# Optimization experiments

Hardware: AMD Instinct MI355X
Metric: run time of the kernel (lower is better)

## Reference

```python
import jax, jax.numpy as jnp
import numpy as np
from jax import lax

VOCAB = 28996  # bert-base-cased vocab size (static for segment_sum)
B, S, D = 32, 512, 768
NUM_CLASSES = 9


def _lstm_dir(x, w_ih, w_hh, b_ih, b_hh):
    # x: [T, N, In]; torch gate order i, f, g, o packed along dim 0 of weights
    T, N, _ = x.shape
    H = w_hh.shape[1]
    xg = jnp.einsum('tni,gi->tng', x, w_ih) + b_ih  # precompute input projections [T,N,4H]

    def step(carry, xg_t):
        h, c = carry
        g = xg_t + h @ w_hh.T + b_hh
        i, f, gg, o = jnp.split(g, 4, axis=-1)
        c = jax.nn.sigmoid(f) * c + jax.nn.sigmoid(i) * jnp.tanh(gg)
        h = jax.nn.sigmoid(o) * jnp.tanh(c)
        return (h, c), h

    h0 = jnp.zeros((N, H), x.dtype)
    _, ys = lax.scan(step, (h0, h0), xg)
    return ys  # [T, N, H]


def setup_inputs() -> dict:
    key = jax.random.key(0)
    ks = jax.random.split(key, 8)
    H, In = D, 2 * D
    w = 0.02
    return {
        'batch': jax.random.randint(ks[0], (B, S), 0, VOCAB),
        'hidden': jax.random.normal(ks[1], (B, S, D), jnp.float32),
        'w_ih_f': jax.random.normal(ks[2], (4 * H, In), jnp.float32) * w,
        'w_hh_f': jax.random.normal(ks[3], (4 * H, H), jnp.float32) * w,
        'b_ih_f': jnp.zeros((4 * H,), jnp.float32),
        'b_hh_f': jnp.zeros((4 * H,), jnp.float32),
        'w_ih_b': jax.random.normal(ks[4], (4 * H, In), jnp.float32) * w,
        'w_hh_b': jax.random.normal(ks[5], (4 * H, H), jnp.float32) * w,
        'b_ih_b': jnp.zeros((4 * H,), jnp.float32),
        'b_hh_b': jnp.zeros((4 * H,), jnp.float32),
        'lin_w': jax.random.normal(ks[6], (NUM_CLASSES, 2 * H), jnp.float32) * w,
        'lin_b': jnp.zeros((NUM_CLASSES,), jnp.float32),
    }


def reference(batch, hidden, w_ih_f, w_hh_f, b_ih_f, b_hh_f,
              w_ih_b, w_hh_b, b_ih_b, b_hh_b, lin_w, lin_b):
    b, s, d = hidden.shape
    flat_ids = batch.reshape(-1)            # [B*S]
    flat_h = hidden.reshape(-1, d)          # [B*S, D]
    # segment mean of embeddings grouped by raw token id (the dict loop in torch)
    sums = jax.ops.segment_sum(flat_h, flat_ids, num_segments=VOCAB)
    counts = jax.ops.segment_sum(jnp.ones((flat_ids.shape[0], 1), hidden.dtype),
                                 flat_ids, num_segments=VOCAB)
    means = sums / jnp.maximum(counts, 1.0)
    ctx = means[flat_ids].reshape(b, s, d)  # gather-broadcast back per position
    x = jnp.concatenate([hidden, ctx], axis=2)  # [B, S, 2D]
    # nn.LSTM is not batch_first: scans over dim0 (B acts as time, S as batch)
    out_f = _lstm_dir(x, w_ih_f, w_hh_f, b_ih_f, b_hh_f)
    out_b = _lstm_dir(x[::-1], w_ih_b, w_hh_b, b_ih_b, b_hh_b)[::-1]
    out = jnp.concatenate([out_f, out_b], axis=-1)  # [B, S, 2D]
    # dropout is identity in eval mode
    return out @ lin_w.T + lin_b  # [B, S, num_classes]
```

## Files before the change

### kernel.cpp

```cpp
#include <hip/hip_runtime.h>

#define VOCAB 28996
#define BB 32
#define SS 512
#define DD 768
#define NCLS 9
#define ROWS (BB*SS)
#define IN2 (2*DD)
#define G4 (4*DD)
#define NB2 (2*G4)

typedef __attribute__((ext_vector_type(8))) short short8;
typedef __attribute__((ext_vector_type(4))) short shortx4;
typedef __attribute__((ext_vector_type(4))) float floatx4;
typedef unsigned long long ull;

__device__ __forceinline__ float bf2f(unsigned short u){
  union { unsigned int i; float f; } v; v.i = ((unsigned int)u) << 16; return v.f;
}
__device__ __forceinline__ unsigned short f2bf(float f){
  union { float f; unsigned int i; } v; v.f = f;
  unsigned int r = v.i + 0x7FFFu + ((v.i >> 16) & 1u);
  return (unsigned short)(r >> 16);
}
__device__ __forceinline__ float sigf(float x){ return 1.0f / (1.0f + __expf(-x)); }
__device__ __forceinline__ float tanhfast(float x){
  float y = fminf(fmaxf(x, -15.f), 15.f);
  float e = __expf(2.f * y);
  return 1.f - 2.f / (e + 1.f);
}

__device__ __forceinline__ void gl_lds16(const unsigned short* g, unsigned short* l){
  __builtin_amdgcn_global_load_lds((__attribute__((address_space(1))) void*)(g),
                                   (__attribute__((address_space(3))) void*)(l), 16, 0, 0);
}
__device__ __forceinline__ void gl_lds16_c(const unsigned short* g, unsigned short* l){
  __builtin_amdgcn_global_load_lds((__attribute__((address_space(1))) void*)(g),
                                   (__attribute__((address_space(3))) void*)(l), 16, 0, 17);
}
__device__ __forceinline__ void store16_sc1(unsigned short* p, short8 v){
  asm volatile("global_store_dwordx4 %0, %1, off sc0 sc1" :: "v"(p), "v"(v) : "memory");
}

#define VMCNT(n) do { asm volatile("s_waitcnt vmcnt(" #n ")" ::: "memory"); \
                      __builtin_amdgcn_sched_barrier(0); } while (0)

__global__ void seg_scatter(const int* __restrict__ ids, const float* __restrict__ hidden,
                            float* __restrict__ sums, float* __restrict__ counts)
{
  int r = blockIdx.x;
  int id = ids[r];
  const float* h = hidden + (long)r * DD;
  float* s = sums + (long)id * DD;
  for (int d = threadIdx.x; d < DD; d += 256)
    atomicAdd(&s[d], h[d]);
  if (threadIdx.x == 0) atomicAdd(&counts[id], 1.0f);
}

__global__ void build_x(const int* __restrict__ ids, const float* __restrict__ hidden,
                        const float* __restrict__ sums, const float* __restrict__ counts,
                        unsigned short* __restrict__ x)
{
  int r = blockIdx.x;
  int id = ids[r];
  float inv = 1.0f / fmaxf(counts[id], 1.0f);
  const float* h = hidden + (long)r * DD;
  const float* s = sums + (long)id * DD;
  unsigned short* xr = x + (long)r * IN2;
  for (int d = threadIdx.x; d < DD; d += 256) {
    xr[d]      = f2bf(h[d]);
    xr[DD + d] = f2bf(s[d] * inv);
  }
}

__global__ void conv_w_perm(const float* __restrict__ w, unsigned short* __restrict__ o, int K)
{
  long i = (long)blockIdx.x * 256 + threadIdx.x;
  if (i >= (long)G4 * K) return;
  int row = (int)(i / K); int k = (int)(i - (long)row * K);
  int u = row >> 2, g = row & 3;
  o[i] = f2bf(w[((long)(g * DD + u)) * K + k]);
}

__global__ void conv_bias_perm(const float* __restrict__ bif, const float* __restrict__ bhf,
                               const float* __restrict__ bib, const float* __restrict__ bhb,
                               float* __restrict__ o)
{
  int n = blockIdx.x * 256 + threadIdx.x;
  if (n >= NB2) return;
  int d = n / G4, rr = n - d * G4, u = rr >> 2, g = rr & 3;
  int s = g * DD + u;
  o[n] = d ? (bib[s] + bhb[s]) : (bif[s] + bhf[s]);
}

__global__ __launch_bounds__(512, 1)
void gemm_bt256(const unsigned short* __restrict__ A, int lda,
                const unsigned short* __restrict__ B, int ldb,
                unsigned short* __restrict__ C, int ldc,
                const float* __restrict__ bias, int K)
{
  __shared__ unsigned short lA[2][16384];
  __shared__ unsigned short lB[2][16384];
  const int t = threadIdx.x;
  const int lane = t & 63;
  const int wv = t >> 6;
  const int wm = wv >> 1;
  const int wn = wv & 1;
  const int l15 = lane & 15, q = lane >> 4;
  const long m0 = (long)blockIdx.x * 256;
  const long n0 = (long)blockIdx.y * 256;
  const int rs  = t >> 2;
  const int sc  = (((t & 3) ^ ((t >> 3) & 3))) * 8;
  const int qsw = (q ^ ((l15 >> 1) & 3)) * 8;

  const unsigned short* gA = A + (m0 + rs) * (long)lda + sc;
  const unsigned short* gB = B + (n0 + rs) * (long)ldb + sc;
  const long a128 = (long)128 * lda;
  const long b128 = (long)128 * ldb;

  #define PIECE(b, kt, p, hf) do {                                               \
    const long kb_ = (long)(kt) * 64 + (p) * 32 + (hf) * 0;                      \
    gl_lds16(gA + kb_ + (hf) * a128, &lA[b][(p) * 8192 + (hf) * 4096 + t * 8]);  \
    gl_lds16(gB + kb_ + (hf) * b128, &lB[b][(p) * 8192 + (hf) * 4096 + t * 8]);  \
  } while (0)

  floatx4 acc[4][8];
  #pragma unroll
  for (int i = 0; i < 4; i++)
    #pragma unroll
    for (int j = 0; j < 8; j++)
      acc[i][j] = (floatx4){0.f, 0.f, 0.f, 0.f};

  PIECE(0, 0, 0, 0); PIECE(0, 0, 0, 1);
  PIECE(0, 0, 1, 0); PIECE(0, 0, 1, 1);

  #pragma unroll 2
  for (int kt = 0; kt < 24; kt++) {
    const int cur = kt & 1;
    const int nxt = cur ^ 1;
    const unsigned short* pA = &lA[cur][0];
    const unsigned short* pB = &lB[cur][0];

    VMCNT(4);
    __builtin_amdgcn_s_barrier();

    #pragma unroll
    for (int ks = 0; ks < 2; ks++) {
      short8 bfr[8];
      #pragma unroll
      for (int ih = 0; ih < 2; ih++) {
        if (kt < 23) {
          if (ks == 0 && ih == 0) PIECE(nxt, kt + 1, 0, 0);
          if (ks == 0 && ih == 1) PIECE(nxt, kt + 1, 0, 1);
          if (ks == 1 && ih == 0) PIECE(nxt, kt + 1, 1, 0);
          if (ks == 1 && ih == 1) PIECE(nxt, kt + 1, 1, 1);
        }
        if (ih == 0) {
          #pragma unroll
          for (int j = 0; j < 8; j++)
            bfr[j] = *(const short8*)(pB + ks * 8192 + (wn * 128 + j * 16 + l15) * 32 + qsw);
        }
        short8 af[2];
        #pragma unroll
        for (int ii = 0; ii < 2; ii++)
          af[ii] = *(const short8*)(pA + ks * 8192 + (wm * 64 + (ih * 2 + ii) * 16 + l15) * 32 + qsw);
        __builtin_amdgcn_s_setprio(1);
        #pragma unroll
        for (int ii = 0; ii < 2; ii++)
          #pragma unroll
          for (int j = 0; j < 8; j++)
            acc[ih * 2 + ii][j] =
              __builtin_amdgcn_mfma_f32_16x16x32_bf16(af[ii], bfr[j], acc[ih * 2 + ii][j], 0, 0, 0);
        __builtin_amdgcn_s_setprio(0);
      }
      if (ks == 0) {
        if (kt < 23) VMCNT(4); else VMCNT(0);
        __builtin_amdgcn_s_barrier();
      }
    }
  }
  #undef PIECE

  #pragma unroll
  for (int i = 0; i < 4; i++) {
    #pragma unroll
    for (int j = 0; j < 8; j++) {
      const long mg = m0 + wm * 64 + i * 16 + q * 4;
      const long ng = n0 + wn * 128 + j * 16 + l15;
      const float bb = bias[ng];
      #pragma unroll
      for (int r = 0; r < 4; r++)
        C[(mg + r) * (long)ldc + ng] = f2bf(acc[i][j][r] + bb);
    }
  }
}

__global__ __launch_bounds__(512, 1)
void lstm_persist(const unsigned short* __restrict__ xg, int ldxg,
                  const unsigned short* __restrict__ whh,
                  unsigned short* __restrict__ hbuf,
                  unsigned short* __restrict__ outc,
                  unsigned* bar,
                  int dir0, int ndir)
{
  __shared__ unsigned short bufA[2][16384];
  __shared__ unsigned short bufB[2][16384];
  __shared__ unsigned short hout[128 * 40];

  const int bid = blockIdx.x;
  const int xcd = bid & 7;
  const int idx = bid >> 3;
  int dm, k3;
  if (ndir == 2) { dm = idx & 7; k3 = idx >> 3; }
  else           { dm = idx & 3; k3 = idx >> 2; }
  const int ld  = (ndir == 2) ? (dm & 1) : 0;
  const int dir = dir0 + ld;
  const int mt  = (ndir == 2) ? (dm >> 1) : dm;
  const int nt  = k3 * 8 + xcd;
  const int m0 = mt * 128, n0 = nt * 128;
  const int u0 = n0 >> 2;
  unsigned* gbar = bar + dm * 16;
  const int nb24 = 24;

  const int t0 = threadIdx.x;
  const int lane = t0 & 63;
  const int wv = t0 >> 6;
  const int wm = wv >> 1;
  const int wn = wv & 1;
  const int l15 = lane & 15, q = lane >> 4;
  const long ldoff = (ndir == 2 && ld == 1) ? (long)G4 : 0;

  const unsigned short* Bdir = whh + (long)dir * G4 * DD;
  const int srow  = lane >> 2;
  const int scolA = (((lane & 3) ^ ((lane >> 3) & 3))) * 8;
  const int qsw   = (q ^ ((l15 >> 1) & 3)) * 8;

  const int rb = wv * 16 + srow;
  const unsigned short* wB  = Bdir + (long)(n0 + rb) * DD + scolA;
  const unsigned short* hA0 = hbuf + ((long)0 * ndir + ld) * ((long)SS * DD) + (long)(m0 + rb) * DD + scolA;
  const unsigned short* hA1 = hbuf + ((long)1 * ndir + ld) * ((long)SS * DD) + (long)(m0 + rb) * DD + scolA;

  float c_reg[2][4];
  #pragma unroll
  for (int i = 0; i < 2; i++)
    #pragma unroll
    for (int j = 0; j < 4; j++)
      c_reg[i][j] = 0.f;

  for (int s = 0; s < BB; s++) {
    const int tt = dir ? (BB - 1 - s) : s;
    const unsigned short* hA = (s & 1) ? hA1 : hA0;
    unsigned short* hw = hbuf + (((long)((s + 1) & 1)) * ndir + ld) * ((long)SS * DD);

    #pragma unroll
    for (int p = 0; p < 4; p++) {
      gl_lds16_c(hA + p * 32, &bufA[0][p * 4096 + wv * 512 + lane * 8]);
      gl_lds16 (wB + p * 32, &bufB[0][p * 4096 + wv * 512 + lane * 8]);
    }
    shortx4 xr0[4], xr1[4];
    {
      const unsigned short* xb = xg + ((long)tt * SS + m0) * ldxg + ldoff + n0;
      const unsigned short* xb0 = xb + (long)(wm * 32 + l15) * ldxg + wn * 64 + q * 4;
      const unsigned short* xb1 = xb0 + (long)16 * ldxg;
      #pragma unroll
      for (int j = 0; j < 4; j++) {
        xr0[j] = *(const shortx4*)(xb0 + j * 16);
        xr1[j] = *(const shortx4*)(xb1 + j * 16);
      }
    }

    floatx4 acc[2][4];
    #pragma unroll
    for (int i = 0; i < 2; i++)
      #pragma unroll
      for (int j = 0; j < 4; j++)
        acc[i][j] = (floatx4){0.f, 0.f, 0.f, 0.f};

    #pragma unroll
    for (int j6 = 0; j6 < 6; j6++) {
      if (j6 < 5) {
        const int b = (j6 + 1) & 1;
        const long kb = (long)(j6 + 1) * 128;
        #pragma unroll
        for (int p = 0; p < 4; p++) {
          gl_lds16_c(hA + kb + p * 32, &bufA[b][p * 4096 + wv * 512 + lane * 8]);
          gl_lds16 (wB + kb + p * 32, &bufB[b][p * 4096 + wv * 512 + lane * 8]);
        }
      }
      if (j6 == 0)      VMCNT(16);
      else if (j6 < 5)  VMCNT(8);
      else              VMCNT(0);
      __builtin_amdgcn_s_barrier();
      const int b = j6 & 1;
      __builtin_amdgcn_s_setprio(1);
      #pragma unroll
      for (int ks = 0; ks < 4; ks++) {
        const unsigned short* pA = &bufA[b][ks * 4096];
        const unsigned short* pB = &bufB[b][ks * 4096];
        short8 af[2], bfr[4];
        #pragma unroll
        for (int i = 0; i < 2; i++)
          af[i] = *(const short8*)(pA + (wm * 32 + i * 16 + l15) * 32 + qsw);
        #pragma unroll
        for (int j = 0; j < 4; j++)
          bfr[j] = *(const short8*)(pB + (wn * 64 + j * 16 + l15) * 32 + qsw);
        #pragma unroll
        for (int i = 0; i < 2; i++)
          #pragma unroll
          for (int j = 0; j < 4; j++)
            acc[i][j] = __builtin_amdgcn_mfma_f32_16x16x32_bf16(bfr[j], af[i], acc[i][j], 0, 0, 0);
      }
      __builtin_amdgcn_s_setprio(0);
      if (j6 < 5) __builtin_amdgcn_s_barrier();
    }

    #pragma unroll
    for (int i = 0; i < 2; i++) {
      const int mrow = wm * 32 + i * 16 + l15;
      #pragma unroll
      for (int j = 0; j < 4; j++) {
        const int nb = wn * 64 + j * 16 + q * 4;
        shortx4 xv = i ? xr1[j] : xr0[j];
        float gi = acc[i][j][0] + bf2f((unsigned short)xv[0]);
        float gf = acc[i][j][1] + bf2f((unsigned short)xv[1]);
        float gg = acc[i][j][2] + bf2f((unsigned short)xv[2]);
        float go = acc[i][j][3] + bf2f((unsigned short)xv[3]);
        float c = sigf(gf) * c_reg[i][j] + sigf(gi) * tanhfast(gg);
        float h = sigf(go) * tanhfast(c);
        c_reg[i][j] = c;
        hout[mrow * 40 + (nb >> 2)] = f2bf(h);
      }
    }
    __syncthreads();
    {
      const int row = t0 >> 2;
      const int qq = t0 & 3;
      short8 v0 = *(const short8*)(hout + row * 40 + qq * 8);
      unsigned short* hwp = hw + (long)(m0 + row) * DD + u0 + qq * 8;
      unsigned short* op  = outc + ((long)tt * SS + m0 + row) * IN2 + dir * DD + u0 + qq * 8;
      store16_sc1(hwp, v0);
      *(short8*)op = v0;
    }
    if (s < BB - 1) {
      VMCNT(0);
      __builtin_amdgcn_s_barrier();
      if (threadIdx.x == 0) {
        unsigned g = __hip_atomic_load(gbar + 1, __ATOMIC_RELAXED, __HIP_MEMORY_SCOPE_AGENT);
        unsigned a = __hip_atomic_fetch_add(gbar, 1u, __ATOMIC_RELAXED, __HIP_MEMORY_SCOPE_AGENT);
        if (a == (unsigned)(nb24 - 1)) {
          __hip_atomic_store(gbar, 0u, __ATOMIC_RELAXED, __HIP_MEMORY_SCOPE_AGENT);
          __hip_atomic_store(gbar + 1, g + 1u, __ATOMIC_RELEASE, __HIP_MEMORY_SCOPE_AGENT);
        } else {
          unsigned curv;
          do {
            __builtin_amdgcn_s_sleep(2);
            curv = __hip_atomic_load(gbar + 1, __ATOMIC_RELAXED, __HIP_MEMORY_SCOPE_AGENT);
          } while (curv == g);
        }
      }
      __builtin_amdgcn_s_barrier();
    }
  }
}

__global__ void final_linear(const unsigned short* __restrict__ xin, const float* __restrict__ w,
                             const float* __restrict__ b, float* __restrict__ out)
{
  __shared__ float red[NCLS * 256];
  int row = blockIdx.x;
  const unsigned short* x = xin + (long)row * IN2;
  float p[NCLS];
  #pragma unroll
  for (int c = 0; c < NCLS; c++) p[c] = 0.f;
  for (int k = threadIdx.x; k < IN2; k += 256) {
    float xv = bf2f(x[k]);
    #pragma unroll
    for (int c = 0; c < NCLS; c++) p[c] += xv * w[c * IN2 + k];
  }
  #pragma unroll
  for (int c = 0; c < NCLS; c++) red[c * 256 + threadIdx.x] = p[c];
  __syncthreads();
  for (int s = 128; s > 0; s >>= 1) {
    if (threadIdx.x < s) {
      #pragma unroll
      for (int c = 0; c < NCLS; c++)
        red[c * 256 + threadIdx.x] += red[c * 256 + threadIdx.x + s];
    }
    __syncthreads();
  }
  if (threadIdx.x < NCLS)
    out[(long)row * NCLS + threadIdx.x] = red[threadIdx.x * 256] + b[threadIdx.x];
}

extern "C" void kernel_launch(void* const* d_in, const int* in_sizes, int n_in,
                              void* d_out, int out_size, void* d_ws, size_t ws_size,
                              hipStream_t stream)
{
  const int*   batch  = (const int*)d_in[0];
  const float* hidden = (const float*)d_in[1];
  const float* w_ih_f = (const float*)d_in[2];
  const float* w_hh_f = (const float*)d_in[3];
  const float* b_ih_f = (const float*)d_in[4];
  const float* b_hh_f = (const float*)d_in[5];
  const float* w_ih_b = (const float*)d_in[6];
  const float* w_hh_b = (const float*)d_in[7];
  const float* b_ih_b = (const float*)d_in[8];
  const float* b_hh_b = (const float*)d_in[9];
  const float* lin_w  = (const float*)d_in[10];
  const float* lin_b  = (const float*)d_in[11];
  float* out = (float*)d_out;

  char* ws = (char*)d_ws;
  size_t off = 0;
  auto alloc = [&](size_t bytes) -> char* {
    char* p = ws + off;
    off += (bytes + 255) & ~(size_t)255;
    return p;
  };

  const size_t SZ_XG_A = (size_t)ROWS * NB2 * 2;
  const size_t SZ_XG_B = (size_t)ROWS * G4  * 2;
  const size_t SZ_XBF  = (size_t)ROWS * IN2 * 2;
  const size_t SZ_W    = (size_t)G4 * IN2 * 2;
  const size_t SZ_BIAS = (size_t)NB2 * 4;
  const size_t SZ_HBUF = (size_t)2 * 2 * SS * DD * 2;
  const size_t SZ_BAR  = 512;
  const size_t SZ_SUMS = (size_t)VOCAB * DD * 4 + (size_t)VOCAB * 4;

  const size_t NEED_C = SZ_XG_A + SZ_XBF + SZ_W + SZ_BIAS + SZ_HBUF + SZ_BAR + 8 * 256;
  const bool combined = ws_size >= NEED_C;

  const long nWIH = (long)G4 * IN2;
  const long nWHH = (long)G4 * DD;

  if (combined) {
    unsigned short* xg   = (unsigned short*)alloc(SZ_XG_A);
    unsigned short* xbf  = (unsigned short*)alloc(SZ_XBF);
    unsigned short* wbuf = (unsigned short*)alloc(SZ_W);
    float*          bias = (float*)alloc(SZ_BIAS);
    unsigned short* hbuf = (unsigned short*)alloc(SZ_HBUF);
    unsigned*       bar  = (unsigned*)alloc(SZ_BAR);
    float* sums   = (float*)xg;
    float* counts = sums + (size_t)VOCAB * DD;

    hipMemsetAsync(sums, 0, SZ_SUMS, stream);
    hipMemsetAsync(bar, 0, SZ_BAR, stream);
    seg_scatter<<<ROWS, 256, 0, stream>>>(batch, hidden, sums, counts);
    build_x<<<ROWS, 256, 0, stream>>>(batch, hidden, sums, counts, xbf);
    conv_bias_perm<<<(NB2 + 255) / 256, 256, 0, stream>>>(b_ih_f, b_hh_f, b_ih_b, b_hh_b, bias);

    for (int dir = 0; dir < 2; dir++) {
      conv_w_perm<<<(unsigned)((nWIH + 255) / 256), 256, 0, stream>>>(dir ? w_ih_b : w_ih_f, wbuf, IN2);
      dim3 grid(ROWS / 256, G4 / 256, 1);
      gemm_bt256<<<grid, 512, 0, stream>>>(xbf, IN2, wbuf, IN2,
                                           xg + (size_t)dir * G4, NB2,
                                           bias + (size_t)dir * G4, IN2);
    }
    conv_w_perm<<<(unsigned)((nWHH + 255) / 256), 256, 0, stream>>>(w_hh_f, wbuf, DD);
    conv_w_perm<<<(unsigned)((nWHH + 255) / 256), 256, 0, stream>>>(w_hh_b, wbuf + (size_t)G4 * DD, DD);

    hipMemsetAsync(hbuf, 0, SZ_HBUF, stream);
    lstm_persist<<<192, 512, 0, stream>>>(xg, NB2, wbuf, hbuf, xbf, bar, 0, 2);
    final_linear<<<ROWS, 256, 0, stream>>>(xbf, lin_w, lin_b, out);
  } else {
    unsigned short* xg   = (unsigned short*)alloc(SZ_XG_B);
    unsigned short* xbf  = (unsigned short*)alloc(SZ_XBF);
    unsigned short* outc = (unsigned short*)alloc(SZ_XBF);
    unsigned short* wih  = (unsigned short*)alloc(SZ_W);
    unsigned short* whh  = (unsigned short*)alloc(SZ_W);
    float*          bias = (float*)alloc(SZ_BIAS);
    unsigned short* hbuf = (unsigned short*)alloc(SZ_HBUF);
    unsigned*       bar  = (unsigned*)alloc(SZ_BAR);
    float* sums   = (float*)xg;
    float* counts = sums + (size_t)VOCAB * DD;

    hipMemsetAsync(sums, 0, SZ_SUMS, stream);
    hipMemsetAsync(bar, 0, SZ_BAR, stream);
    seg_scatter<<<ROWS, 256, 0, stream>>>(batch, hidden, sums, counts);
    build_x<<<ROWS, 256, 0, stream>>>(batch, hidden, sums, counts, xbf);
    conv_bias_perm<<<(NB2 + 255) / 256, 256, 0, stream>>>(b_ih_f, b_hh_f, b_ih_b, b_hh_b, bias);
    conv_w_perm<<<(unsigned)((nWHH + 255) / 256), 256, 0, stream>>>(w_hh_f, whh, DD);
    conv_w_perm<<<(unsigned)((nWHH + 255) / 256), 256, 0, stream>>>(w_hh_b, whh + (size_t)G4 * DD, DD);

    for (int dir = 0; dir < 2; dir++) {
      conv_w_perm<<<(unsigned)((nWIH + 255) / 256), 256, 0, stream>>>(dir ? w_ih_b : w_ih_f, wih, IN2);
      {
        dim3 grid(ROWS / 256, G4 / 256, 1);
        gemm_bt256<<<grid, 512, 0, stream>>>(xbf, IN2, wih, IN2, xg, G4,
                                             bias + (size_t)dir * G4, IN2);
      }
      hipMemsetAsync(hbuf, 0, SZ_HBUF, stream);
      lstm_persist<<<96, 512, 0, stream>>>(xg, G4, whh, hbuf, outc, bar, dir, 1);
    }
    final_linear<<<ROWS, 256, 0, stream>>>(outc, lin_w, lin_b, out);
  }
}
```

Baseline: 1.169 ms.

## Place each LSTM barrier group on one XCD and use local-coherent h traffic

For the two-direction persistent LSTM launch, blocks are remapped so that every block sharing a barrier group (same dm) lands on the same XCD, given round-robin block dispatch. The h-state loads then use a cache policy that is not system-coherent, and the h-state stores drop the sc0/sc1 bypass, so exchange between blocks can stay in the XCD-local L2. This relies on the hardware assigning blocks to XCDs round-robin. If that placement does not hold, the non-coherent reads could see stale h values.

Measured after the change: 1.136 ms. 1.03x faster.

```diff
diff --git a/kernel.cpp b/kernel.cpp
--- a/kernel.cpp
+++ b/kernel.cpp
@@ -34,9 +34,11 @@
   __builtin_amdgcn_global_load_lds((__attribute__((address_space(1))) void*)(g),
                                    (__attribute__((address_space(3))) void*)(l), 16, 0, 0);
 }
-__device__ __forceinline__ void gl_lds16_c(const unsigned short* g, unsigned short* l){
+template<int LOCAL>
+__device__ __forceinline__ void gl_lds16_h(const unsigned short* g, unsigned short* l){
   __builtin_amdgcn_global_load_lds((__attribute__((address_space(1))) void*)(g),
-                                   (__attribute__((address_space(3))) void*)(l), 16, 0, 17);
+                                   (__attribute__((address_space(3))) void*)(l), 16, 0,
+                                   LOCAL ? 1 : 17);
 }
 __device__ __forceinline__ void store16_sc1(unsigned short* p, short8 v){
   asm volatile("global_store_dwordx4 %0, %1, off sc0 sc1" :: "v"(p), "v"(v) : "memory");
@@ -119,7 +121,7 @@
   const long b128 = (long)128 * ldb;
 
   #define PIECE(b, kt, p, hf) do {                                               \
-    const long kb_ = (long)(kt) * 64 + (p) * 32 + (hf) * 0;                      \
+    const long kb_ = (long)(kt) * 64 + (p) * 32;                                 \
     gl_lds16(gA + kb_ + (hf) * a128, &lA[b][(p) * 8192 + (hf) * 4096 + t * 8]);  \
     gl_lds16(gB + kb_ + (hf) * b128, &lB[b][(p) * 8192 + (hf) * 4096 + t * 8]);  \
   } while (0)
@@ -195,6 +197,7 @@
   }
 }
 
+template<int LOCAL>
 __global__ __launch_bounds__(512, 1)
 void lstm_persist(const unsigned short* __restrict__ xg, int ldxg,
                   const unsigned short* __restrict__ whh,
@@ -208,15 +211,13 @@
   __shared__ unsigned short hout[128 * 40];
 
   const int bid = blockIdx.x;
-  const int xcd = bid & 7;
-  const int idx = bid >> 3;
-  int dm, k3;
-  if (ndir == 2) { dm = idx & 7; k3 = idx >> 3; }
-  else           { dm = idx & 3; k3 = idx >> 2; }
+  int dm, nt;
+  if (LOCAL) { dm = bid & 7; nt = bid >> 3; }
+  else { int xcd = bid & 7; int idx = bid >> 3;
+         dm = idx & 3; nt = (idx >> 2) * 8 + xcd; }
   const int ld  = (ndir == 2) ? (dm & 1) : 0;
   const int dir = dir0 + ld;
   const int mt  = (ndir == 2) ? (dm >> 1) : dm;
-  const int nt  = k3 * 8 + xcd;
   const int m0 = mt * 128, n0 = nt * 128;
   const int u0 = n0 >> 2;
   unsigned* gbar = bar + dm * 16;
@@ -254,8 +255,8 @@
 
     #pragma unroll
     for (int p = 0; p < 4; p++) {
-      gl_lds16_c(hA + p * 32, &bufA[0][p * 4096 + wv * 512 + lane * 8]);
-      gl_lds16 (wB + p * 32, &bufB[0][p * 4096 + wv * 512 + lane * 8]);
+      gl_lds16_h<LOCAL>(hA + p * 32, &bufA[0][p * 4096 + wv * 512 + lane * 8]);
+      gl_lds16         (wB + p * 32, &bufB[0][p * 4096 + wv * 512 + lane * 8]);
     }
     shortx4 xr0[4], xr1[4];
     {
@@ -283,8 +284,8 @@
         const long kb = (long)(j6 + 1) * 128;
         #pragma unroll
         for (int p = 0; p < 4; p++) {
-          gl_lds16_c(hA + kb + p * 32, &bufA[b][p * 4096 + wv * 512 + lane * 8]);
-          gl_lds16 (wB + kb + p * 32, &bufB[b][p * 4096 + wv * 512 + lane * 8]);
+          gl_lds16_h<LOCAL>(hA + kb + p * 32, &bufA[b][p * 4096 + wv * 512 + lane * 8]);
+          gl_lds16         (wB + kb + p * 32, &bufB[b][p * 4096 + wv * 512 + lane * 8]);
         }
       }
       if (j6 == 0)      VMCNT(16);
@@ -338,7 +339,8 @@
       short8 v0 = *(const short8*)(hout + row * 40 + qq * 8);
       unsigned short* hwp = hw + (long)(m0 + row) * DD + u0 + qq * 8;
       unsigned short* op  = outc + ((long)tt * SS + m0 + row) * IN2 + dir * DD + u0 + qq * 8;
-      store16_sc1(hwp, v0);
+      if (LOCAL) *(short8*)hwp = v0;
+      else       store16_sc1(hwp, v0);
       *(short8*)op = v0;
     }
     if (s < BB - 1) {
@@ -460,7 +462,7 @@
     conv_w_perm<<<(unsigned)((nWHH + 255) / 256), 256, 0, stream>>>(w_hh_b, wbuf + (size_t)G4 * DD, DD);
 
     hipMemsetAsync(hbuf, 0, SZ_HBUF, stream);
-    lstm_persist<<<192, 512, 0, stream>>>(xg, NB2, wbuf, hbuf, xbf, bar, 0, 2);
+    lstm_persist<1><<<192, 512, 0, stream>>>(xg, NB2, wbuf, hbuf, xbf, bar, 0, 2);
     final_linear<<<ROWS, 256, 0, stream>>>(xbf, lin_w, lin_b, out);
   } else {
     unsigned short* xg   = (unsigned short*)alloc(SZ_XG_B);
@@ -490,7 +492,7 @@
                                              bias + (size_t)dir * G4, IN2);
       }
       hipMemsetAsync(hbuf, 0, SZ_HBUF, stream);
-      lstm_persist<<<96, 512, 0, stream>>>(xg, G4, whh, hbuf, outc, bar, dir, 1);
+      lstm_persist<0><<<96, 512, 0, stream>>>(xg, G4, whh, hbuf, outc, bar, dir, 1);
     }
     final_linear<<<ROWS, 256, 0, stream>>>(outc, lin_w, lin_b, out);
   }
```
